# Kernel tuning notes

Measured on AMD Instinct MI355X. Metric: run time of the kernel, lower is better.

## Reference

```python
import jax, jax.numpy as jnp
import numpy as np

N = 50000
IN_DIM = 512
HIDDEN = 64
OUT_DIM = 47
E1 = 800000
E2 = 1200000


def setup_inputs() -> dict:
    key = jax.random.key(0)
    ks = jax.random.split(key, 10)
    x = jax.random.normal(ks[0], (N, IN_DIM), dtype=jnp.float32)
    src1 = jax.random.randint(ks[1], (E1,), 0, N, dtype=jnp.int32)
    dst1 = jax.random.randint(ks[2], (E1,), 0, N, dtype=jnp.int32)
    w1 = jax.random.uniform(ks[3], (E1,), dtype=jnp.float32)
    src2 = jax.random.randint(ks[4], (E2,), 0, N, dtype=jnp.int32)
    dst2 = jax.random.randint(ks[5], (E2,), 0, N, dtype=jnp.int32)
    w2 = jax.random.uniform(ks[6], (E2,), dtype=jnp.float32)
    embed_w = jax.random.normal(ks[7], (IN_DIM, HIDDEN), dtype=jnp.float32) / np.sqrt(IN_DIM)
    embed_b = jnp.zeros((HIDDEN,), dtype=jnp.float32)
    total_dim = (2 ** 3 - 1) * HIDDEN  # k=2 -> 7*hidden
    cls_w = jax.random.normal(ks[8], (total_dim, OUT_DIM), dtype=jnp.float32) / np.sqrt(total_dim)
    cls_b = jnp.zeros((OUT_DIM,), dtype=jnp.float32)
    return {"x": x, "src1": src1, "dst1": dst1, "w1": w1,
            "src2": src2, "dst2": dst2, "w2": w2,
            "embed_w": embed_w, "embed_b": embed_b,
            "cls_w": cls_w, "cls_b": cls_b}


def _spmm(src, dst, w, h, n):
    # out[i] = sum_{e: dst[e]==i} w[e] * h[src[e]]  == sparse_adj @ h
    return jax.ops.segment_sum(w[:, None] * h[src], dst, num_segments=n)


def reference(x, src1, dst1, w1, src2, dst2, w2, embed_w, embed_b, cls_w, cls_b):
    k = 2
    # dropout is identity in eval mode
    h = jax.nn.relu(x @ embed_w + embed_b)  # [N, hidden]
    reps = [h]
    for _ in range(k):
        h1 = _spmm(src1, dst1, w1, h, N)  # strict 1-hop
        h2 = _spmm(src2, dst2, w2, h, N)  # strict 2-hop
        h = jax.nn.relu(jnp.concatenate([h1, h2], axis=1))
        reps.append(h)
    h_final = jnp.concatenate(reps, axis=1)  # [N, 7*hidden]
    return h_final @ cls_w + cls_b
```

## Files before the change

kernel.cpp:

```cpp
#include <hip/hip_runtime.h>

#define N_NODES 50000
#define IN_DIM 512
#define HIDDEN 64
#define OUT_DIM 47
#define HSTRIDE 448

#define NBINS 391
#define CAP1 3072
#define CAP2 4096
#define CHUNK 4096

typedef unsigned short u16;
typedef short v8s __attribute__((ext_vector_type(8)));
typedef float v4f __attribute__((ext_vector_type(4)));

union F4 { float4 v; float f[4]; };
union U4 { uint4 v; unsigned u[4]; };

static __device__ __forceinline__ u16 f2bf(float f) {
  unsigned u = __float_as_uint(f);
  u += 0x7fffu + ((u >> 16) & 1u);
  return (u16)(u >> 16);
}
static __device__ __forceinline__ float bf2f(u16 h) {
  return __uint_as_float(((unsigned)h) << 16);
}

__global__ __launch_bounds__(256) void prep_scatter(
    const float* __restrict__ embed_w, u16* __restrict__ weTh,
    u16* __restrict__ weTl, const float* __restrict__ cls_w,
    u16* __restrict__ wcTh, u16* __restrict__ wcTl,
    const int* __restrict__ src1, const int* __restrict__ dst1,
    const float* __restrict__ w1, int E1, int c1,
    const int* __restrict__ src2, const int* __restrict__ dst2,
    const float* __restrict__ w2, int E2,
    int* __restrict__ binCursor, int2* __restrict__ stg1,
    int2* __restrict__ stg2) {
  int b = blockIdx.x;
  if (b < 16) {
    int tid = b * 256 + threadIdx.x;
    int col = tid >> 6;
    int k8 = (tid & 63) * 8;
#pragma unroll
    for (int j = 0; j < 8; j++) {
      float v = embed_w[(size_t)(k8 + j) * HIDDEN + col];
      u16 h = f2bf(v);
      weTh[(size_t)col * IN_DIM + k8 + j] = h;
      weTl[(size_t)col * IN_DIM + k8 + j] = f2bf(v - bf2f(h));
    }
    return;
  }
  if (b < 27) {
    int tid = (b - 16) * 256 + threadIdx.x;
    if (tid < 48 * 56) {
      int col = tid / 56;
      int k8 = (tid % 56) * 8;
#pragma unroll
      for (int j = 0; j < 8; j++) {
        float v = (col < OUT_DIM) ? cls_w[(size_t)(k8 + j) * OUT_DIM + col] : 0.f;
        u16 h = f2bf(v);
        wcTh[(size_t)col * HSTRIDE + k8 + j] = h;
        wcTl[(size_t)col * HSTRIDE + k8 + j] = f2bf(v - bf2f(h));
      }
    }
    return;
  }

  int q = b - 27;
  const int *src, *dst;
  const float* w;
  int E, cap;
  int2* stg;
  int* bc;
  if (q < c1) {
    src = src1; dst = dst1; w = w1; E = E1; stg = stg1; bc = binCursor; cap = CAP1;
  } else {
    q -= c1;
    src = src2; dst = dst2; w = w2; E = E2; stg = stg2; bc = binCursor + NBINS; cap = CAP2;
  }
  int e0 = q * CHUNK;
  int n = E - e0;
  if (n > CHUNK) n = CHUNK;

  __shared__ int hist[NBINS], segrel[NBINS], cur[NBINS];
  for (int i = threadIdx.x; i < NBINS; i += 256) { hist[i] = 0; cur[i] = 0; }
  __syncthreads();
  for (int t = threadIdx.x; t < n; t += 256)
    atomicAdd(&hist[dst[e0 + t] >> 7], 1);
  __syncthreads();
  for (int i = threadIdx.x; i < NBINS; i += 256) {
    int h = hist[i];
    segrel[i] = h ? atomicAdd(&bc[i], h) : 0;
  }
  __syncthreads();
  for (int t = threadIdx.x; t < n; t += 256) {
    int d = dst[e0 + t];
    int bin = d >> 7;
    int rel = segrel[bin] + atomicAdd(&cur[bin], 1);
    if (rel < cap)
      stg[(size_t)bin * cap + rel] =
          make_int2(src[e0 + t] | ((d & 127) << 16), __float_as_int(w[e0 + t]));
  }
}

__global__ __launch_bounds__(512) void binscan(const int* __restrict__ cnt,
                                               int* __restrict__ scanout) {
  const int* in = cnt + blockIdx.x * NBINS;
  int* out = scanout + blockIdx.x * NBINS;
  int tid = threadIdx.x, lane = tid & 63, wid = tid >> 6;
  __shared__ int wsum[8];
  int v0 = (tid < NBINS) ? in[tid] : 0;
  int v = v0;
#pragma unroll
  for (int off = 1; off < 64; off <<= 1) {
    int t = __shfl_up(v, off, 64);
    if (lane >= off) v += t;
  }
  if (lane == 63) wsum[wid] = v;
  __syncthreads();
  if (tid < 8) {
    int s = wsum[tid], sc = s;
#pragma unroll
    for (int off = 1; off < 8; off <<= 1) {
      int t = __shfl_up(sc, off, 8);
      if (tid >= off) sc += t;
    }
    wsum[tid] = sc - s;
  }
  __syncthreads();
  if (tid < NBINS) out[tid] = v - v0 + wsum[wid];
}

__global__ __launch_bounds__(256) void embed_place(
    const float* __restrict__ x, const u16* __restrict__ wTh,
    const u16* __restrict__ wTl, const float* __restrict__ bias,
    u16* __restrict__ hcat, const int* __restrict__ binCursor,
    const int* __restrict__ binScan, const int2* __restrict__ stg1,
    int2* __restrict__ ew1, int* __restrict__ ep1,
    const int2* __restrict__ stg2, int2* __restrict__ ew2,
    int* __restrict__ ep2) {
  int b = blockIdx.x;
  if (b < 782) {
    int wave = threadIdx.x >> 6, lane = threadIdx.x & 63;
    int row0 = b * 64 + wave * 16;
    int m = lane & 15, kq = lane >> 4;
    int rowA = row0 + m;
    if (rowA >= N_NODES) rowA = N_NODES - 1;
    const float* xr = x + (size_t)rowA * IN_DIM;

    v4f acc[4];
#pragma unroll
    for (int nf = 0; nf < 4; nf++) acc[nf] = (v4f){0.f, 0.f, 0.f, 0.f};

#pragma unroll 2
    for (int k0 = 0; k0 < IN_DIM; k0 += 32) {
      int kk = k0 + kq * 8;
      F4 p, qv;
      p.v = *(const float4*)(xr + kk);
      qv.v = *(const float4*)(xr + kk + 4);
      v8s ah, al;
#pragma unroll
      for (int j = 0; j < 4; j++) {
        u16 h = f2bf(p.f[j]);
        ah[j] = (short)h;
        al[j] = (short)f2bf(p.f[j] - bf2f(h));
      }
#pragma unroll
      for (int j = 0; j < 4; j++) {
        u16 h = f2bf(qv.f[j]);
        ah[4 + j] = (short)h;
        al[4 + j] = (short)f2bf(qv.f[j] - bf2f(h));
      }
#pragma unroll
      for (int nf = 0; nf < 4; nf++) {
        int col = nf * 16 + m;
        v8s bh = *(const v8s*)(wTh + (size_t)col * IN_DIM + kk);
        v8s bl = *(const v8s*)(wTl + (size_t)col * IN_DIM + kk);
        acc[nf] = __builtin_amdgcn_mfma_f32_16x16x32_bf16(ah, bh, acc[nf], 0, 0, 0);
        acc[nf] = __builtin_amdgcn_mfma_f32_16x16x32_bf16(al, bh, acc[nf], 0, 0, 0);
        acc[nf] = __builtin_amdgcn_mfma_f32_16x16x32_bf16(ah, bl, acc[nf], 0, 0, 0);
      }
    }

#pragma unroll
    for (int nf = 0; nf < 4; nf++) {
      int col = nf * 16 + m;
      float bv = bias[col];
#pragma unroll
      for (int reg = 0; reg < 4; reg++) {
        int rowC = row0 + kq * 4 + reg;
        if (rowC < N_NODES) {
          float v = acc[nf][reg] + bv;
          hcat[(size_t)rowC * HSTRIDE + col] = f2bf(v > 0.f ? v : 0.f);
        }
      }
    }
    return;
  }

  int bin = b - 782;
  int lb = bin < NBINS ? bin : bin - NBINS;
  const int2* stg;
  int2* ew;
  int* ep;
  int cap;
  if (bin < NBINS) { stg = stg1; ew = ew1; ep = ep1; cap = CAP1; }
  else             { stg = stg2; ew = ew2; ep = ep2; cap = CAP2; }
  int cnt = binCursor[bin];
  if (cnt > cap) cnt = cap;
  int base = binScan[bin];
  const int2* seg = stg + (size_t)lb * cap;
  int node0 = lb << 7;
  int nnodes = N_NODES - node0;
  if (nnodes > 128) nnodes = 128;

  __shared__ int ncnt[128], noff[128], ncur[128];
  __shared__ int t0;
  if (threadIdx.x < 128) { ncnt[threadIdx.x] = 0; ncur[threadIdx.x] = 0; }
  __syncthreads();
  for (int t = threadIdx.x; t < cnt; t += 256)
    atomicAdd(&ncnt[(seg[t].x >> 16) & 127], 1);
  __syncthreads();
  int v0 = 0, v = 0;
  if (threadIdx.x < 128) {
    v0 = ncnt[threadIdx.x];
    v = v0;
    int lane = threadIdx.x & 63;
#pragma unroll
    for (int off = 1; off < 64; off <<= 1) {
      int t = __shfl_up(v, off, 64);
      if (lane >= off) v += t;
    }
    if (threadIdx.x == 63) t0 = v;
  }
  __syncthreads();
  if (threadIdx.x < 128) {
    int excl = v - v0 + (threadIdx.x >= 64 ? t0 : 0);
    noff[threadIdx.x] = excl;
    if (threadIdx.x < nnodes) ep[node0 + threadIdx.x] = base + excl + v0;
  }
  __syncthreads();
  for (int t = threadIdx.x; t < cnt; t += 256) {
    int2 pk = seg[t];
    int nl = (pk.x >> 16) & 127;
    int pos = base + noff[nl] + atomicAdd(&ncur[nl], 1);
    ew[pos] = make_int2(pk.x & 0xFFFF, pk.y);
  }
}

__device__ __forceinline__ void bf8_fma(const U4& r, float wt, float* a) {
#pragma unroll
  for (int i = 0; i < 4; i++) {
    a[2 * i]     += wt * __uint_as_float(r.u[i] << 16);
    a[2 * i + 1] += wt * __uint_as_float(r.u[i] & 0xffff0000u);
  }
}

template <int NT>
__global__ __launch_bounds__(256) void gather2(
    const int* __restrict__ ep1, const int2* __restrict__ ew1,
    const int* __restrict__ ep2, const int2* __restrict__ ew2,
    const u16* __restrict__ hin, u16* __restrict__ out1,
    u16* __restrict__ out2, int half_blocks) {
  int b = blockIdx.x;
  const int* ep;
  const int2* ew;
  u16* out;
  if (b < half_blocks) { ep = ep1; ew = ew1; out = out1; }
  else { b -= half_blocks; ep = ep2; ew = ew2; out = out2; }

  int tid = b * 256 + threadIdx.x;
  int node = tid / NT;
  if (node >= N_NODES) return;
  int col0 = (tid % NT) * 8;
  int s = node ? ep[node - 1] : 0;
  int e = ep[node];

  float a0[8], a1[8];
#pragma unroll
  for (int i = 0; i < 8; i++) { a0[i] = 0.f; a1[i] = 0.f; }

  int j = s;
  for (; j + 4 <= e; j += 4) {
    int2 p0 = ew[j], p1 = ew[j + 1], p2 = ew[j + 2], p3 = ew[j + 3];
    U4 r0, r1, r2, r3;
    r0.v = *(const uint4*)(hin + (size_t)p0.x * HSTRIDE + col0);
    r1.v = *(const uint4*)(hin + (size_t)p1.x * HSTRIDE + col0);
    r2.v = *(const uint4*)(hin + (size_t)p2.x * HSTRIDE + col0);
    r3.v = *(const uint4*)(hin + (size_t)p3.x * HSTRIDE + col0);
    bf8_fma(r0, __int_as_float(p0.y), a0);
    bf8_fma(r1, __int_as_float(p1.y), a1);
    bf8_fma(r2, __int_as_float(p2.y), a0);
    bf8_fma(r3, __int_as_float(p3.y), a1);
  }
  for (; j < e; j++) {
    int2 p = ew[j];
    U4 r;
    r.v = *(const uint4*)(hin + (size_t)p.x * HSTRIDE + col0);
    bf8_fma(r, __int_as_float(p.y), a0);
  }

  U4 o;
#pragma unroll
  for (int i = 0; i < 4; i++) {
    float lo = a0[2 * i] + a1[2 * i];
    float hi = a0[2 * i + 1] + a1[2 * i + 1];
    lo = lo > 0.f ? lo : 0.f;
    hi = hi > 0.f ? hi : 0.f;
    o.u[i] = ((unsigned)f2bf(hi) << 16) | (unsigned)f2bf(lo);
  }
  *(uint4*)(out + (size_t)node * HSTRIDE + col0) = o.v;
}

__global__ __launch_bounds__(256) void final_mfma(
    const u16* __restrict__ hcat, const u16* __restrict__ wTh,
    const u16* __restrict__ wTl, const float* __restrict__ bias,
    float* __restrict__ out) {
  int wave = threadIdx.x >> 6, lane = threadIdx.x & 63;
  int row0 = blockIdx.x * 64 + wave * 16;
  int m = lane & 15, kq = lane >> 4;
  int rowA = row0 + m;
  if (rowA >= N_NODES) rowA = N_NODES - 1;
  const u16* hr = hcat + (size_t)rowA * HSTRIDE;

  v4f acc[3];
#pragma unroll
  for (int nf = 0; nf < 3; nf++) acc[nf] = (v4f){0.f, 0.f, 0.f, 0.f};

#pragma unroll 2
  for (int k0 = 0; k0 < HSTRIDE; k0 += 32) {
    int kk = k0 + kq * 8;
    v8s a = *(const v8s*)(hr + kk);
#pragma unroll
    for (int nf = 0; nf < 3; nf++) {
      int col = nf * 16 + m;
      v8s bh = *(const v8s*)(wTh + (size_t)col * HSTRIDE + kk);
      v8s bl = *(const v8s*)(wTl + (size_t)col * HSTRIDE + kk);
      acc[nf] = __builtin_amdgcn_mfma_f32_16x16x32_bf16(a, bh, acc[nf], 0, 0, 0);
      acc[nf] = __builtin_amdgcn_mfma_f32_16x16x32_bf16(a, bl, acc[nf], 0, 0, 0);
    }
  }

#pragma unroll
  for (int nf = 0; nf < 3; nf++) {
    int col = nf * 16 + m;
    if (col < OUT_DIM) {
      float bv = bias[col];
#pragma unroll
      for (int reg = 0; reg < 4; reg++) {
        int rowC = row0 + kq * 4 + reg;
        if (rowC < N_NODES)
          out[(size_t)rowC * OUT_DIM + col] = acc[nf][reg] + bv;
      }
    }
  }
}

extern "C" void kernel_launch(void* const* d_in, const int* in_sizes, int n_in,
                              void* d_out, int out_size, void* d_ws,
                              size_t ws_size, hipStream_t stream) {
  const float* x       = (const float*)d_in[0];
  const int*   src1    = (const int*)d_in[1];
  const int*   dst1    = (const int*)d_in[2];
  const float* w1      = (const float*)d_in[3];
  const int*   src2    = (const int*)d_in[4];
  const int*   dst2    = (const int*)d_in[5];
  const float* w2      = (const float*)d_in[6];
  const float* embed_w = (const float*)d_in[7];
  const float* embed_b = (const float*)d_in[8];
  const float* cls_w   = (const float*)d_in[9];
  const float* cls_b   = (const float*)d_in[10];
  int E1 = in_sizes[1];
  int E2 = in_sizes[4];

  float* ws = (float*)d_ws;
  size_t off = 0;
  u16* hcat = (u16*)(ws + off); off += (size_t)N_NODES * HSTRIDE / 2;
  int2* ew1 = (int2*)(ws + off); off += (size_t)2 * E1;
  int2* ew2 = (int2*)(ws + off); off += (size_t)2 * E2;
  int* ep1 = (int*)(ws + off); off += N_NODES;
  int* ep2 = (int*)(ws + off); off += N_NODES;
  int2* stg1 = (int2*)(ws + off); off += (size_t)2 * NBINS * CAP1;
  int2* stg2 = (int2*)(ws + off); off += (size_t)2 * NBINS * CAP2;
  int* binCursor = (int*)(ws + off); off += 2 * NBINS;
  int* binScan = (int*)(ws + off); off += 2 * NBINS;
  u16* weTh = (u16*)(ws + off); off += 16384;
  u16* weTl = (u16*)(ws + off); off += 16384;
  u16* wcTh = (u16*)(ws + off); off += 10752;
  u16* wcTl = (u16*)(ws + off); off += 10752;

  int c1 = (E1 + CHUNK - 1) / CHUNK;
  int c2 = (E2 + CHUNK - 1) / CHUNK;

  hipMemsetAsync(binCursor, 0, 2 * NBINS * sizeof(int), stream);
  prep_scatter<<<27 + c1 + c2, 256, 0, stream>>>(
      embed_w, weTh, weTl, cls_w, wcTh, wcTl,
      src1, dst1, w1, E1, c1, src2, dst2, w2, E2,
      binCursor, stg1, stg2);
  binscan<<<2, 512, 0, stream>>>(binCursor, binScan);
  embed_place<<<782 + 2 * NBINS, 256, 0, stream>>>(
      x, weTh, weTl, embed_b, hcat, binCursor, binScan,
      stg1, ew1, ep1, stg2, ew2, ep2);
  gather2<8><<<3126, 256, 0, stream>>>(ep1, ew1, ep2, ew2, hcat,
                                       hcat + 64, hcat + 128, 1563);
  gather2<16><<<6250, 256, 0, stream>>>(ep1, ew1, ep2, ew2, hcat + 64,
                                        hcat + 192, hcat + 320, 3125);
  final_mfma<<<782, 256, 0, stream>>>(hcat, wcTh, wcTl, cls_b, (float*)d_out);
}
```

Baseline: 261.1 us.

## Pre-convert x to bf16 in prep kernel and restructure gathers into column slices

Adds a grid-stride pass inside the prep kernel that converts x to bf16 once. The embedding GEMM then reads half the bytes and issues two MFMAs per tile instead of three, dropping the low-part correction for x. The gather kernels are rewritten so each block handles a 32-column slice of one adjacency, with 4 threads per node. This is meant to improve L2 locality on the hcat rows. The cost is an extra 50 MB read and write pass for the conversion, lower precision on x, and a fallback path used when the workspace is too small.

After: 380.4 us. 45.7% more time.

```diff
diff --git a/kernel.cpp b/kernel.cpp
--- a/kernel.cpp
+++ b/kernel.cpp
@@ -10,6 +10,7 @@
 #define CAP1 3072
 #define CAP2 4096
 #define CHUNK 4096
+#define XCONV_BLKS 1536
 
 typedef unsigned short u16;
 typedef short v8s __attribute__((ext_vector_type(8)));
@@ -31,6 +32,7 @@
     const float* __restrict__ embed_w, u16* __restrict__ weTh,
     u16* __restrict__ weTl, const float* __restrict__ cls_w,
     u16* __restrict__ wcTh, u16* __restrict__ wcTl,
+    const float* __restrict__ x, u16* __restrict__ x_bf, int xb,
     const int* __restrict__ src1, const int* __restrict__ dst1,
     const float* __restrict__ w1, int E1, int c1,
     const int* __restrict__ src2, const int* __restrict__ dst2,
@@ -66,8 +68,24 @@
     }
     return;
   }
-
-  int q = b - 27;
+  if (b < 27 + xb) {
+    const float4* x4 = (const float4*)x;
+    uint2* o2 = (uint2*)x_bf;
+    int i0 = (b - 27) * 256 + threadIdx.x;
+    int stride = xb * 256;
+    int tot = N_NODES * IN_DIM / 4;
+    for (int i = i0; i < tot; i += stride) {
+      F4 v;
+      v.v = x4[i];
+      uint2 o;
+      o.x = (unsigned)f2bf(v.f[0]) | ((unsigned)f2bf(v.f[1]) << 16);
+      o.y = (unsigned)f2bf(v.f[2]) | ((unsigned)f2bf(v.f[3]) << 16);
+      o2[i] = o;
+    }
+    return;
+  }
+
+  int q = b - 27 - xb;
   const int *src, *dst;
   const float* w;
   int E, cap;
@@ -132,14 +150,15 @@
   if (tid < NBINS) out[tid] = v - v0 + wsum[wid];
 }
 
+template <bool PRE>
 __global__ __launch_bounds__(256) void embed_place(
-    const float* __restrict__ x, const u16* __restrict__ wTh,
-    const u16* __restrict__ wTl, const float* __restrict__ bias,
-    u16* __restrict__ hcat, const int* __restrict__ binCursor,
-    const int* __restrict__ binScan, const int2* __restrict__ stg1,
-    int2* __restrict__ ew1, int* __restrict__ ep1,
-    const int2* __restrict__ stg2, int2* __restrict__ ew2,
-    int* __restrict__ ep2) {
+    const float* __restrict__ x, const u16* __restrict__ x_bf,
+    const u16* __restrict__ wTh, const u16* __restrict__ wTl,
+    const float* __restrict__ bias, u16* __restrict__ hcat,
+    const int* __restrict__ binCursor, const int* __restrict__ binScan,
+    const int2* __restrict__ stg1, int2* __restrict__ ew1,
+    int* __restrict__ ep1, const int2* __restrict__ stg2,
+    int2* __restrict__ ew2, int* __restrict__ ep2) {
   int b = blockIdx.x;
   if (b < 782) {
     int wave = threadIdx.x >> 6, lane = threadIdx.x & 63;
@@ -147,39 +166,56 @@
     int m = lane & 15, kq = lane >> 4;
     int rowA = row0 + m;
     if (rowA >= N_NODES) rowA = N_NODES - 1;
-    const float* xr = x + (size_t)rowA * IN_DIM;
 
     v4f acc[4];
 #pragma unroll
     for (int nf = 0; nf < 4; nf++) acc[nf] = (v4f){0.f, 0.f, 0.f, 0.f};
 
+    if constexpr (PRE) {
+      const u16* xr = x_bf + (size_t)rowA * IN_DIM;
+#pragma unroll 4
+      for (int k0 = 0; k0 < IN_DIM; k0 += 32) {
+        int kk = k0 + kq * 8;
+        v8s a = *(const v8s*)(xr + kk);
+#pragma unroll
+        for (int nf = 0; nf < 4; nf++) {
+          int col = nf * 16 + m;
+          v8s bh = *(const v8s*)(wTh + (size_t)col * IN_DIM + kk);
+          v8s bl = *(const v8s*)(wTl + (size_t)col * IN_DIM + kk);
+          acc[nf] = __builtin_amdgcn_mfma_f32_16x16x32_bf16(a, bh, acc[nf], 0, 0, 0);
+          acc[nf] = __builtin_amdgcn_mfma_f32_16x16x32_bf16(a, bl, acc[nf], 0, 0, 0);
+        }
+      }
+    } else {
+      const float* xr = x + (size_t)rowA * IN_DIM;
 #pragma unroll 2
-    for (int k0 = 0; k0 < IN_DIM; k0 += 32) {
-      int kk = k0 + kq * 8;
-      F4 p, qv;
-      p.v = *(const float4*)(xr + kk);
-      qv.v = *(const float4*)(xr + kk + 4);
-      v8s ah, al;
-#pragma unroll
-      for (int j = 0; j < 4; j++) {
-        u16 h = f2bf(p.f[j]);
-        ah[j] = (short)h;
-        al[j] = (short)f2bf(p.f[j] - bf2f(h));
-      }
-#pragma unroll
-      for (int j = 0; j < 4; j++) {
-        u16 h = f2bf(qv.f[j]);
-        ah[4 + j] = (short)h;
-        al[4 + j] = (short)f2bf(qv.f[j] - bf2f(h));
-      }
-#pragma unroll
-      for (int nf = 0; nf < 4; nf++) {
-        int col = nf * 16 + m;
-        v8s bh = *(const v8s*)(wTh + (size_t)col * IN_DIM + kk);
-        v8s bl = *(const v8s*)(wTl + (size_t)col * IN_DIM + kk);
-        acc[nf] = __builtin_amdgcn_mfma_f32_16x16x32_bf16(ah, bh, acc[nf], 0, 0, 0);
-        acc[nf] = __builtin_amdgcn_mfma_f32_16x16x32_bf16(al, bh, acc[nf], 0, 0, 0);
-        acc[nf] = __builtin_amdgcn_mfma_f32_16x16x32_bf16(ah, bl, acc[nf], 0, 0, 0);
+      for (int k0 = 0; k0 < IN_DIM; k0 += 32) {
+        int kk = k0 + kq * 8;
+        F4 p, qv;
+        p.v = *(const float4*)(xr + kk);
+        qv.v = *(const float4*)(xr + kk + 4);
+        v8s ah, al;
+#pragma unroll
+        for (int j = 0; j < 4; j++) {
+          u16 h = f2bf(p.f[j]);
+          ah[j] = (short)h;
+          al[j] = (short)f2bf(p.f[j] - bf2f(h));
+        }
+#pragma unroll
+        for (int j = 0; j < 4; j++) {
+          u16 h = f2bf(qv.f[j]);
+          ah[4 + j] = (short)h;
+          al[4 + j] = (short)f2bf(qv.f[j] - bf2f(h));
+        }
+#pragma unroll
+        for (int nf = 0; nf < 4; nf++) {
+          int col = nf * 16 + m;
+          v8s bh = *(const v8s*)(wTh + (size_t)col * IN_DIM + kk);
+          v8s bl = *(const v8s*)(wTl + (size_t)col * IN_DIM + kk);
+          acc[nf] = __builtin_amdgcn_mfma_f32_16x16x32_bf16(ah, bh, acc[nf], 0, 0, 0);
+          acc[nf] = __builtin_amdgcn_mfma_f32_16x16x32_bf16(al, bh, acc[nf], 0, 0, 0);
+          acc[nf] = __builtin_amdgcn_mfma_f32_16x16x32_bf16(ah, bl, acc[nf], 0, 0, 0);
+        }
       }
     }
 
@@ -257,26 +293,26 @@
   }
 }
 
-template <int NT>
-__global__ __launch_bounds__(256) void gather2(
+__global__ __launch_bounds__(256) void gather_cs(
     const int* __restrict__ ep1, const int2* __restrict__ ew1,
     const int* __restrict__ ep2, const int2* __restrict__ ew2,
-    const u16* __restrict__ hin, u16* __restrict__ out1,
-    u16* __restrict__ out2, int half_blocks) {
-  int b = blockIdx.x;
-  const int* ep;
-  const int2* ew;
-  u16* out;
-  if (b < half_blocks) { ep = ep1; ew = ew1; out = out1; }
-  else { b -= half_blocks; ep = ep2; ew = ew2; out = out2; }
-
-  int tid = b * 256 + threadIdx.x;
-  int node = tid / NT;
+    u16* __restrict__ hcat, int in0, int ob1, int ob2) {
+  int seg = blockIdx.x / 782;
+  int bb = blockIdx.x % 782;
+  const int* ep = (seg & 1) ? ep2 : ep1;
+  const int2* ew = (seg & 1) ? ew2 : ew1;
+  int ob = (seg & 1) ? ob2 : ob1;
+  int coff = (seg >> 1) * 32;
+
+  int t = bb * 256 + threadIdx.x;
+  int node = t >> 2;
   if (node >= N_NODES) return;
-  int col0 = (tid % NT) * 8;
+  int col0 = in0 + coff + (t & 3) * 8;
+  int oc0 = ob + coff + (t & 3) * 8;
   int s = node ? ep[node - 1] : 0;
   int e = ep[node];
 
+  const u16* hin = hcat;
   float a0[8], a1[8];
 #pragma unroll
   for (int i = 0; i < 8; i++) { a0[i] = 0.f; a1[i] = 0.f; }
@@ -310,7 +346,7 @@
     hi = hi > 0.f ? hi : 0.f;
     o.u[i] = ((unsigned)f2bf(hi) << 16) | (unsigned)f2bf(lo);
   }
-  *(uint4*)(out + (size_t)node * HSTRIDE + col0) = o.v;
+  *(uint4*)(hcat + (size_t)node * HSTRIDE + oc0) = o.v;
 }
 
 __global__ __launch_bounds__(256) void final_mfma(
@@ -389,22 +425,28 @@
   u16* weTl = (u16*)(ws + off); off += 16384;
   u16* wcTh = (u16*)(ws + off); off += 10752;
   u16* wcTl = (u16*)(ws + off); off += 10752;
+  u16* x_bf = (u16*)(ws + off); off += (size_t)N_NODES * IN_DIM / 2;
+  bool use_xbf = ws_size >= off * sizeof(float);
+  int xb = use_xbf ? XCONV_BLKS : 0;
 
   int c1 = (E1 + CHUNK - 1) / CHUNK;
   int c2 = (E2 + CHUNK - 1) / CHUNK;
 
   hipMemsetAsync(binCursor, 0, 2 * NBINS * sizeof(int), stream);
-  prep_scatter<<<27 + c1 + c2, 256, 0, stream>>>(
-      embed_w, weTh, weTl, cls_w, wcTh, wcTl,
+  prep_scatter<<<27 + xb + c1 + c2, 256, 0, stream>>>(
+      embed_w, weTh, weTl, cls_w, wcTh, wcTl, x, x_bf, xb,
       src1, dst1, w1, E1, c1, src2, dst2, w2, E2,
       binCursor, stg1, stg2);
   binscan<<<2, 512, 0, stream>>>(binCursor, binScan);
-  embed_place<<<782 + 2 * NBINS, 256, 0, stream>>>(
-      x, weTh, weTl, embed_b, hcat, binCursor, binScan,
-      stg1, ew1, ep1, stg2, ew2, ep2);
-  gather2<8><<<3126, 256, 0, stream>>>(ep1, ew1, ep2, ew2, hcat,
-                                       hcat + 64, hcat + 128, 1563);
-  gather2<16><<<6250, 256, 0, stream>>>(ep1, ew1, ep2, ew2, hcat + 64,
-                                        hcat + 192, hcat + 320, 3125);
+  if (use_xbf)
+    embed_place<true><<<782 + 2 * NBINS, 256, 0, stream>>>(
+        x, x_bf, weTh, weTl, embed_b, hcat, binCursor, binScan,
+        stg1, ew1, ep1, stg2, ew2, ep2);
+  else
+    embed_place<false><<<782 + 2 * NBINS, 256, 0, stream>>>(
+        x, x_bf, weTh, weTl, embed_b, hcat, binCursor, binScan,
+        stg1, ew1, ep1, stg2, ew2, ep2);
+  gather_cs<<<4 * 782, 256, 0, stream>>>(ep1, ew1, ep2, ew2, hcat, 0, 64, 128);
+  gather_cs<<<8 * 782, 256, 0, stream>>>(ep1, ew1, ep2, ew2, hcat, 64, 192, 320);
   final_mfma<<<782, 256, 0, stream>>>(hcat, wcTh, wcTl, cls_b, (float*)d_out);
 }
```
